# Kernel tuning notes

Hardware: AMD Instinct MI355X
Metric: run time of the kernel (lower is better)

## Reference

```python
import jax, jax.numpy as jnp
import numpy as np

K = 3

def setup_inputs() -> dict:
    key = jax.random.key(0)
    k1, k2, k3, k4 = jax.random.split(key, 4)
    B, N, F_in, T, F_out = 8, 2048, 16, 12, 32
    x = jax.random.normal(k1, (B, N, F_in, T), dtype=jnp.float32)
    spatial_attention = jax.random.uniform(k2, (B, N, N), dtype=jnp.float32)
    node_embeddings = jax.random.normal(k3, (N, 16), dtype=jnp.float32)
    theta = jax.random.normal(k4, (K, F_in, F_out), dtype=jnp.float32) * 0.1
    return {"x": x, "spatial_attention": spatial_attention,
            "node_embeddings": node_embeddings, "theta": theta}

def _cheb_polys(node_embeddings, N, K):
    # supports = softmax(relu(E E^T), axis=1)
    supports = jax.nn.softmax(jax.nn.relu(node_embeddings @ node_embeddings.T), axis=1)
    polys = [jnp.eye(N, dtype=supports.dtype), supports]
    for _ in range(2, K):
        polys.append(2.0 * supports @ polys[-1] - polys[-2])
    return jnp.stack(polys[:K], axis=0)  # (K, N, N)

def reference(x, spatial_attention, node_embeddings, theta):
    B, N, F_in, T = x.shape
    polys = _cheb_polys(node_embeddings, N, K)             # (K,N,N)
    # T_k_with_at = polys[k] * attention (broadcast over batch);
    # rhs = T_k_with_at^T @ graph_signal for every timestep:
    # (K,N,N)*(B,N,N) contracted with (B,N,F,T) over source node n -> (K,B,M,F,T)
    rhs = jnp.einsum('knm,bnm,bnft->kbmft', polys, spatial_attention, x)
    # accumulate rhs @ theta_k over k -> (B,M,F_out,T)
    out = jnp.einsum('kbmft,kfo->bmot', rhs, theta)
    return jax.nn.relu(out)
```

## Files before the change

### kernel.cpp

```cpp
#include <hip/hip_runtime.h>

#define NN    2048
#define BATCH 8
#define FIN   16
#define TT    12
#define FOUT  32
#define FT    (FIN*TT)
#define OT    (FOUT*TT)

typedef unsigned short ushort_t;
typedef __attribute__((ext_vector_type(8))) short   short8;
typedef __attribute__((ext_vector_type(4))) float   f32x4;
typedef __attribute__((ext_vector_type(4))) unsigned short us4;
typedef __attribute__((ext_vector_type(8))) unsigned short us8;

__device__ __forceinline__ float b2f(unsigned short u) {
    union { unsigned int i; float f; } v; v.i = ((unsigned int)u) << 16; return v.f;
}
__device__ __forceinline__ unsigned short f2b(float f) {
    union { float f; unsigned int i; } v; v.f = f;
    unsigned int x = v.i;
    x += 0x7fffu + ((x >> 16) & 1u);
    return (unsigned short)(x >> 16);
}

__global__ __launch_bounds__(256)
void k_supports(const float* __restrict__ E, ushort_t* __restrict__ Sb) {
    const int n = blockIdx.x;
    __shared__ float row[NN];
    __shared__ float red[256];
    const int tid = threadIdx.x;

    const f32x4 en0 = *(const f32x4*)&E[n * 16 + 0];
    const f32x4 en1 = *(const f32x4*)&E[n * 16 + 4];
    const f32x4 en2 = *(const f32x4*)&E[n * 16 + 8];
    const f32x4 en3 = *(const f32x4*)&E[n * 16 + 12];

    float lmax = 0.0f;
    for (int m = tid; m < NN; m += 256) {
        const f32x4* Em = (const f32x4*)&E[(size_t)m * 16];
        const f32x4 e0 = Em[0], e1 = Em[1], e2 = Em[2], e3 = Em[3];
        float d = 0.0f;
        #pragma unroll
        for (int j = 0; j < 4; ++j) d += en0[j] * e0[j];
        #pragma unroll
        for (int j = 0; j < 4; ++j) d += en1[j] * e1[j];
        #pragma unroll
        for (int j = 0; j < 4; ++j) d += en2[j] * e2[j];
        #pragma unroll
        for (int j = 0; j < 4; ++j) d += en3[j] * e3[j];
        d = fmaxf(d, 0.0f);
        row[m] = d;
        lmax = fmaxf(lmax, d);
    }
    red[tid] = lmax; __syncthreads();
    for (int s = 128; s > 0; s >>= 1) {
        if (tid < s) red[tid] = fmaxf(red[tid], red[tid + s]);
        __syncthreads();
    }
    const float mx = red[0];
    __syncthreads();

    float lsum = 0.0f;
    for (int m = tid; m < NN; m += 256) {
        float e = __expf(row[m] - mx);
        row[m] = e;
        lsum += e;
    }
    red[tid] = lsum; __syncthreads();
    for (int s = 128; s > 0; s >>= 1) {
        if (tid < s) red[tid] += red[tid + s];
        __syncthreads();
    }
    const float inv = 1.0f / red[0];
    for (int m = tid; m < NN; m += 256) Sb[(size_t)n * NN + m] = f2b(row[m] * inv);
}

__global__ __launch_bounds__(256)
void k_pack_st(const ushort_t* __restrict__ Sb, ushort_t* __restrict__ SbT) {
    const int r0 = blockIdx.x * 64, c0 = blockIdx.y * 64;
    __shared__ ushort_t Lt[64][65];
    const int tid = threadIdx.x;
    #pragma unroll
    for (int p = 0; p < 2; ++p) {
        const int i = (tid >> 3) + p * 32;
        const int j8 = (tid & 7) * 8;
        us8 v = *(const us8*)&Sb[(size_t)(r0 + i) * NN + c0 + j8];
        #pragma unroll
        for (int e = 0; e < 8; ++e) Lt[i][j8 + e] = v[e];
    }
    __syncthreads();
    #pragma unroll
    for (int p = 0; p < 2; ++p) {
        const int jj = (tid >> 3) + p * 32;
        const int i8 = (tid & 7) * 8;
        us8 v;
        #pragma unroll
        for (int e = 0; e < 8; ++e) v[e] = Lt[i8 + e][jj];
        *(us8*)&SbT[(size_t)(c0 + jj) * NN + r0 + i8] = v;
    }
}

__global__ __launch_bounds__(256)
void k_pack_x(const float* __restrict__ x, ushort_t* __restrict__ xbT) {
    const int nc = blockIdx.x * 64;
    const int b  = blockIdx.y;
    __shared__ ushort_t Lt[FT][65];
    const int tid = threadIdx.x;
    const float* __restrict__ xb = x + (size_t)b * NN * FT;
    #pragma unroll
    for (int p = 0; p < 12; ++p) {
        const int id = tid + 256 * p;
        const int nn = id / 48;
        const int f4 = (id % 48) * 4;
        const float4 v = *(const float4*)&xb[(size_t)(nc + nn) * FT + f4];
        Lt[f4 + 0][nn] = f2b(v.x);
        Lt[f4 + 1][nn] = f2b(v.y);
        Lt[f4 + 2][nn] = f2b(v.z);
        Lt[f4 + 3][nn] = f2b(v.w);
    }
    __syncthreads();
    #pragma unroll
    for (int p = 0; p < 6; ++p) {
        const int id = tid + 256 * p;
        const int ft = id >> 3;
        const int n8 = (id & 7) * 8;
        us8 v;
        #pragma unroll
        for (int e = 0; e < 8; ++e) v[e] = Lt[ft][n8 + e];
        *(us8*)&xbT[((size_t)b * FT + ft) * NN + nc + n8] = v;
    }
}

__global__ __launch_bounds__(256, 4)
void k_t2(const ushort_t* __restrict__ Sb, const ushort_t* __restrict__ SbT,
          ushort_t* __restrict__ T2b) {
    const int m0 = blockIdx.x * 64;
    const int n0 = blockIdx.y * 64;
    __shared__ __align__(16) ushort_t As[2][64 * 64];
    __shared__ __align__(16) ushort_t Bs[2][64 * 64];
    const int tid = threadIdx.x;
    const int lane = tid & 63, w = tid >> 6;
    const int l15 = lane & 15, q = lane >> 4, l7 = lane & 7;
    const int n0w = (w & 1) * 32, m0w = (w >> 1) * 32;
    const int sr = tid >> 3;
    const int sc = tid & 7;

    f32x4 acc[2][2];
    #pragma unroll
    for (int i = 0; i < 2; ++i)
        #pragma unroll
        for (int j = 0; j < 2; ++j) acc[i][j] = {0.f, 0.f, 0.f, 0.f};

    us8 avA[2], bvA[2], avB[2], bvB[2];

#define T2_LOAD(l0, av, bv)                                              \
    { _Pragma("unroll") for (int p = 0; p < 2; ++p) {                    \
        const int row_ = sr + 32 * p;                                    \
        av[p] = *(const us8*)&Sb[(size_t)(n0 + row_) * NN + (l0) + sc * 8];  \
        bv[p] = *(const us8*)&SbT[(size_t)(m0 + row_) * NN + (l0) + sc * 8]; \
      } }

#define T2_STORE(bufi, av, bv)                                           \
    { _Pragma("unroll") for (int p = 0; p < 2; ++p) {                    \
        const int row_ = sr + 32 * p;                                    \
        const int cs_ = (sc ^ (row_ & 7)) * 8;                           \
        *(us8*)&As[bufi][row_ * 64 + cs_] = av[p];                       \
        *(us8*)&Bs[bufi][row_ * 64 + cs_] = bv[p];                       \
      } }

#define T2_MFMA(bufi)                                                    \
    { _Pragma("unroll") for (int s = 0; s < 2; ++s) {                    \
        short8 a_[2], b_[2];                                             \
        const int u_ = ((s * 4 + q) ^ l7) * 8;                           \
        _Pragma("unroll") for (int i = 0; i < 2; ++i)                    \
            a_[i] = *(const short8*)&As[bufi][(n0w + i * 16 + l15) * 64 + u_]; \
        _Pragma("unroll") for (int j = 0; j < 2; ++j)                    \
            b_[j] = *(const short8*)&Bs[bufi][(m0w + j * 16 + l15) * 64 + u_]; \
        _Pragma("unroll") for (int i = 0; i < 2; ++i)                    \
            _Pragma("unroll") for (int j = 0; j < 2; ++j)                \
                acc[i][j] = __builtin_amdgcn_mfma_f32_16x16x32_bf16(a_[i], b_[j], acc[i][j], 0, 0, 0); \
      } }

    T2_LOAD(0, avA, bvA);
    T2_LOAD(64, avB, bvB);
    T2_STORE(0, avA, bvA);

    for (int it = 0; it < 32; it += 2) {
        __syncthreads();
        if (it < 30) T2_LOAD((it + 2) * 64, avA, bvA);
        T2_MFMA(0);
        T2_STORE(1, avB, bvB);
        __syncthreads();
        if (it < 29) T2_LOAD((it + 3) * 64, avB, bvB);
        T2_MFMA(1);
        if (it < 30) T2_STORE(0, avA, bvA);
    }
#undef T2_LOAD
#undef T2_STORE
#undef T2_MFMA

    #pragma unroll
    for (int i = 0; i < 2; ++i)
        #pragma unroll
        for (int j = 0; j < 2; ++j)
            #pragma unroll
            for (int r = 0; r < 4; ++r) {
                const int ng = n0 + n0w + i * 16 + q * 4 + r;
                const int mg = m0 + m0w + j * 16 + l15;
                const float v = 2.0f * acc[i][j][r] - (ng == mg ? 1.0f : 0.0f);
                T2b[(size_t)ng * NN + mg] = f2b(v);
            }
}

__global__ __launch_bounds__(256, 2)
void k_rhs(const ushort_t* __restrict__ Sb, const ushort_t* __restrict__ T2b,
           const float* __restrict__ att, const ushort_t* __restrict__ xbT,
           float* __restrict__ rhs) {
    const int m0 = blockIdx.x * 32;
    const int b  = blockIdx.y;
    __shared__ __align__(16) ushort_t As[2][2 * 32 * 64];
    __shared__ __align__(16) ushort_t Xs[2][FT * 64];
    const int tid = threadIdx.x;
    const int lane = tid & 63, w = tid >> 6;
    const int l15 = lane & 15, q = lane >> 4, l7 = lane & 7, l3 = lane >> 3;
    const int k1 = w & 1, ft0 = (w >> 1) * 96;
    const float* __restrict__ attb = att + (size_t)b * NN * NN;

    const int k1s = tid >> 7;
    const int uu  = tid & 127;
    const int m4  = (uu & 7) * 4;
    const int nn4 = (uu >> 3) * 4;
    const ushort_t* __restrict__ Pk = k1s ? T2b : Sb;

    f32x4 acc[2][6];
    #pragma unroll
    for (int i = 0; i < 2; ++i)
        #pragma unroll
        for (int t = 0; t < 6; ++t) acc[i][t] = {0.f, 0.f, 0.f, 0.f};

    us8   xvA[6], xvB[6];
    us4   pvA[4], pvB[4];
    f32x4 avA[4], avB[4];

#define RHS_LOAD(nc, xv, pv, av)                                         \
    { _Pragma("unroll") for (int p = 0; p < 6; ++p) {                    \
        const int row_ = (w * 6 + p) * 8 + l3;                           \
        xv[p] = *(const us8*)&xbT[((size_t)b * FT + row_) * NN + (nc) + l7 * 8]; \
      }                                                                  \
      _Pragma("unroll") for (int r = 0; r < 4; ++r) {                    \
        const int nn_ = (nc) + nn4 + r;                                  \
        pv[r] = *(const us4*)&Pk[(size_t)nn_ * NN + m0 + m4];            \
        av[r] = *(const f32x4*)&attb[(size_t)nn_ * NN + m0 + m4];        \
      } }

#define RHS_STORE(bufi, xv, pv, av)                                      \
    { _Pragma("unroll") for (int p = 0; p < 6; ++p) {                    \
        const int row_ = (w * 6 + p) * 8 + l3;                           \
        *(us8*)&Xs[bufi][row_ * 64 + (l7 ^ l3) * 8] = xv[p];             \
      }                                                                  \
      _Pragma("unroll") for (int c = 0; c < 4; ++c) {                    \
        const float w0_ = b2f(pv[0][c]) * av[0][c];                      \
        const float w1_ = b2f(pv[1][c]) * av[1][c];                      \
        const float w2_ = b2f(pv[2][c]) * av[2][c];                      \
        const float w3_ = b2f(pv[3][c]) * av[3][c];                      \
        unsigned int u01_, u23_;                                         \
        asm("v_cvt_pk_bf16_f32 %0, %1, %2" : "=v"(u01_) : "v"(w0_), "v"(w1_)); \
        asm("v_cvt_pk_bf16_f32 %0, %1, %2" : "=v"(u23_) : "v"(w2_), "v"(w3_)); \
        const int rowm_ = m4 + c;                                        \
        const int off_ = (((nn4 >> 3) ^ (rowm_ & 7)) * 8) + (nn4 & 4);   \
        *(uint2*)&As[bufi][(k1s * 32 + rowm_) * 64 + off_] = make_uint2(u01_, u23_); \
      } }

#define RHS_MFMA(bufi)                                                   \
    { _Pragma("unroll") for (int s = 0; s < 2; ++s) {                    \
        short8 a_[2], bb_[6];                                            \
        _Pragma("unroll") for (int i = 0; i < 2; ++i) {                  \
            const int row_ = i * 16 + l15;                               \
            a_[i] = *(const short8*)&As[bufi][(k1 * 32 + row_) * 64 + (((s * 4 + q) ^ l7) * 8)]; \
        }                                                                \
        _Pragma("unroll") for (int t = 0; t < 6; ++t) {                  \
            const int col_ = ft0 + t * 16 + l15;                         \
            const int u_ = ((s * 4 + q) ^ (col_ & 7)) * 8;               \
            bb_[t] = *(const short8*)&Xs[bufi][col_ * 64 + u_];          \
        }                                                                \
        _Pragma("unroll") for (int i = 0; i < 2; ++i)                    \
            _Pragma("unroll") for (int t = 0; t < 6; ++t)                \
                acc[i][t] = __builtin_amdgcn_mfma_f32_16x16x32_bf16(a_[i], bb_[t], acc[i][t], 0, 0, 0); \
      } }

    RHS_LOAD(0, xvA, pvA, avA);
    RHS_LOAD(64, xvB, pvB, avB);
    RHS_STORE(0, xvA, pvA, avA);

    for (int it = 0; it < 32; it += 2) {
        __syncthreads();
        if (it < 30) RHS_LOAD((it + 2) * 64, xvA, pvA, avA);
        RHS_MFMA(0);
        RHS_STORE(1, xvB, pvB, avB);
        __syncthreads();
        if (it < 29) RHS_LOAD((it + 3) * 64, xvB, pvB, avB);
        RHS_MFMA(1);
        if (it < 30) RHS_STORE(0, xvA, pvA, avA);
    }
#undef RHS_LOAD
#undef RHS_STORE
#undef RHS_MFMA

    float* __restrict__ op = rhs + ((size_t)(k1 * BATCH + b)) * NN * FT;
    #pragma unroll
    for (int i = 0; i < 2; ++i)
        #pragma unroll
        for (int t = 0; t < 6; ++t)
            #pragma unroll
            for (int r = 0; r < 4; ++r) {
                const int mg = m0 + i * 16 + q * 4 + r;
                const int ftg = ft0 + t * 16 + l15;
                op[(size_t)mg * FT + ftg] = acc[i][t][r];
            }
}

__global__ __launch_bounds__(128)
void k_out(const float* __restrict__ x, const float* __restrict__ att,
           const float* __restrict__ theta, const float* __restrict__ rhs,
           float* __restrict__ out) {
    const int m = blockIdx.x & (NN - 1);
    const int b = blockIdx.x >> 11;
    __shared__ float xr[FT], r1[FT], r2[FT];
    __shared__ float th[3 * FIN * FOUT];
    const int tid = threadIdx.x;

    const float* __restrict__ xb = x + ((size_t)b * NN + m) * FT;
    const float* __restrict__ p1 = rhs + ((size_t)0 * BATCH + b) * NN * FT + (size_t)m * FT;
    const float* __restrict__ p2 = rhs + ((size_t)1 * BATCH + b) * NN * FT + (size_t)m * FT;
    const float a0 = att[((size_t)b * NN + m) * NN + m];

    for (int i = tid; i < FT; i += 128) {
        xr[i] = xb[i] * a0;
        r1[i] = p1[i];
        r2[i] = p2[i];
    }
    for (int i = tid; i < 3 * FIN * FOUT; i += 128) th[i] = theta[i];
    __syncthreads();

    float* __restrict__ ob = out + ((size_t)b * NN + m) * OT;
    for (int idx = tid; idx < OT; idx += 128) {
        const int o = idx / TT, t = idx % TT;
        float acc = 0.0f;
        #pragma unroll
        for (int f = 0; f < FIN; ++f) {
            const int ft = f * TT + t;
            acc += th[f * FOUT + o] * xr[ft];
            acc += th[512 + f * FOUT + o] * r1[ft];
            acc += th[1024 + f * FOUT + o] * r2[ft];
        }
        ob[idx] = fmaxf(acc, 0.0f);
    }
}

extern "C" void kernel_launch(void* const* d_in, const int* in_sizes, int n_in,
                              void* d_out, int out_size, void* d_ws, size_t ws_size,
                              hipStream_t stream) {
    const float* x     = (const float*)d_in[0];
    const float* att   = (const float*)d_in[1];
    const float* E     = (const float*)d_in[2];
    const float* theta = (const float*)d_in[3];
    float* out = (float*)d_out;

    ushort_t* Sb  = (ushort_t*)d_ws;
    ushort_t* SbT = Sb  + (size_t)NN * NN;
    ushort_t* T2b = SbT + (size_t)NN * NN;
    ushort_t* xbT = T2b + (size_t)NN * NN;
    float*    rhs = (float*)(xbT + (size_t)BATCH * FT * NN);

    k_supports<<<NN, 256, 0, stream>>>(E, Sb);
    k_pack_st<<<dim3(32, 32), 256, 0, stream>>>(Sb, SbT);
    k_pack_x<<<dim3(32, BATCH), 256, 0, stream>>>(x, xbT);
    k_t2<<<dim3(32, 32), 256, 0, stream>>>(Sb, SbT, T2b);
    k_rhs<<<dim3(64, BATCH), 256, 0, stream>>>(Sb, T2b, att, xbT, rhs);
    k_out<<<BATCH * NN, 128, 0, stream>>>(x, att, theta, rhs, out);
}
```

Baseline: 338.7 us.

## Deepen GEMM software pipeline with explicit vmcnt waits and raw barriers

Restructures the double-buffered main loops of the T2 and RHS GEMM kernels so that two global loads stay in flight. The kernels now wait with explicit s_waitcnt vmcnt counts instead of relying on __syncthreads' full waits, and use s_barrier wrapped in sched_barrier. The aim is to overlap global-memory latency with MFMA work more aggressively. The risk is that the hard-coded vmcnt values must exactly match the number of loads each macro issues, or the code will read stale data.

```diff
diff --git a/kernel.cpp b/kernel.cpp
--- a/kernel.cpp
+++ b/kernel.cpp
@@ -23,6 +23,12 @@
     x += 0x7fffu + ((x >> 16) & 1u);
     return (unsigned short)(x >> 16);
 }
+
+#define VMWAIT(n) asm volatile("s_waitcnt vmcnt(" #n ")" ::: "memory")
+#define LGKM0()   asm volatile("s_waitcnt lgkmcnt(0)" ::: "memory")
+#define BAR()     do { __builtin_amdgcn_sched_barrier(0); \
+                       __builtin_amdgcn_s_barrier();      \
+                       __builtin_amdgcn_sched_barrier(0); } while (0)
 
 __global__ __launch_bounds__(256)
 void k_supports(const float* __restrict__ E, ushort_t* __restrict__ Sb) {
@@ -184,18 +190,22 @@
 
     T2_LOAD(0, avA, bvA);
     T2_LOAD(64, avB, bvB);
+    VMWAIT(4);
     T2_STORE(0, avA, bvA);
-
-    for (int it = 0; it < 32; it += 2) {
-        __syncthreads();
-        if (it < 30) T2_LOAD((it + 2) * 64, avA, bvA);
-        T2_MFMA(0);
-        T2_STORE(1, avB, bvB);
-        __syncthreads();
-        if (it < 29) T2_LOAD((it + 3) * 64, avB, bvB);
-        T2_MFMA(1);
-        if (it < 30) T2_STORE(0, avA, bvA);
-    }
+    T2_LOAD(128, avA, bvA);
+    LGKM0(); BAR();
+
+    for (int it = 0; it < 28; it += 2) {
+        T2_MFMA(0); VMWAIT(4); T2_STORE(1, avB, bvB);
+        T2_LOAD((it + 3) * 64, avB, bvB); LGKM0(); BAR();
+        T2_MFMA(1); VMWAIT(4); T2_STORE(0, avA, bvA);
+        T2_LOAD((it + 4) * 64, avA, bvA); LGKM0(); BAR();
+    }
+    T2_MFMA(0); VMWAIT(4); T2_STORE(1, avB, bvB);
+    T2_LOAD(31 * 64, avB, bvB); LGKM0(); BAR();
+    T2_MFMA(1); VMWAIT(4); T2_STORE(0, avA, bvA); LGKM0(); BAR();
+    T2_MFMA(0); VMWAIT(0); T2_STORE(1, avB, bvB); LGKM0(); BAR();
+    T2_MFMA(1);
 #undef T2_LOAD
 #undef T2_STORE
 #undef T2_MFMA
@@ -291,18 +301,22 @@
 
     RHS_LOAD(0, xvA, pvA, avA);
     RHS_LOAD(64, xvB, pvB, avB);
+    VMWAIT(14);
     RHS_STORE(0, xvA, pvA, avA);
-
-    for (int it = 0; it < 32; it += 2) {
-        __syncthreads();
-        if (it < 30) RHS_LOAD((it + 2) * 64, xvA, pvA, avA);
-        RHS_MFMA(0);
-        RHS_STORE(1, xvB, pvB, avB);
-        __syncthreads();
-        if (it < 29) RHS_LOAD((it + 3) * 64, xvB, pvB, avB);
-        RHS_MFMA(1);
-        if (it < 30) RHS_STORE(0, xvA, pvA, avA);
-    }
+    RHS_LOAD(128, xvA, pvA, avA);
+    LGKM0(); BAR();
+
+    for (int it = 0; it < 28; it += 2) {
+        RHS_MFMA(0); VMWAIT(14); RHS_STORE(1, xvB, pvB, avB);
+        RHS_LOAD((it + 3) * 64, xvB, pvB, avB); LGKM0(); BAR();
+        RHS_MFMA(1); VMWAIT(14); RHS_STORE(0, xvA, pvA, avA);
+        RHS_LOAD((it + 4) * 64, xvA, pvA, avA); LGKM0(); BAR();
+    }
+    RHS_MFMA(0); VMWAIT(14); RHS_STORE(1, xvB, pvB, avB);
+    RHS_LOAD(31 * 64, xvB, pvB, avB); LGKM0(); BAR();
+    RHS_MFMA(1); VMWAIT(14); RHS_STORE(0, xvA, pvA, avA); LGKM0(); BAR();
+    RHS_MFMA(0); VMWAIT(0); RHS_STORE(1, xvB, pvB, avB); LGKM0(); BAR();
+    RHS_MFMA(1);
 #undef RHS_LOAD
 #undef RHS_STORE
 #undef RHS_MFMA
```

Result: slower. 348.1 us (+2.8%).

## Widen k_rhs tile to 64 rows, single-buffer A, and use lighter barriers

Applied to the files above, without the earlier changes.

The k_rhs kernel now computes 64 output rows per block instead of 32, so each loaded X tile feeds twice as many MFMAs. The grid halves to 256 blocks. The A operand (polynomial times attention) is single-buffered and the loop is restructured so that A is written, then the next tile's loads are issued, then MFMA runs. Both k_t2 and k_rhs replace __syncthreads with an lgkmcnt wait plus a raw s_barrier. The larger accumulator and launch_bounds of 1 lower occupancy, and with fewer blocks the 256-CU device may be underfilled.

```diff
diff --git a/kernel.cpp b/kernel.cpp
--- a/kernel.cpp
+++ b/kernel.cpp
@@ -23,6 +23,9 @@
     x += 0x7fffu + ((x >> 16) & 1u);
     return (unsigned short)(x >> 16);
 }
+
+#define LGKM0()   asm volatile("s_waitcnt lgkmcnt(0)" ::: "memory")
+#define BARRIER() __builtin_amdgcn_s_barrier()
 
 __global__ __launch_bounds__(256)
 void k_supports(const float* __restrict__ E, ushort_t* __restrict__ Sb) {
@@ -187,11 +190,11 @@
     T2_STORE(0, avA, bvA);
 
     for (int it = 0; it < 32; it += 2) {
-        __syncthreads();
+        LGKM0(); BARRIER();
         if (it < 30) T2_LOAD((it + 2) * 64, avA, bvA);
         T2_MFMA(0);
         T2_STORE(1, avB, bvB);
-        __syncthreads();
+        LGKM0(); BARRIER();
         if (it < 29) T2_LOAD((it + 3) * 64, avB, bvB);
         T2_MFMA(1);
         if (it < 30) T2_STORE(0, avA, bvA);
@@ -213,13 +216,13 @@
             }
 }
 
-__global__ __launch_bounds__(256, 2)
+__global__ __launch_bounds__(256, 1)
 void k_rhs(const ushort_t* __restrict__ Sb, const ushort_t* __restrict__ T2b,
            const float* __restrict__ att, const ushort_t* __restrict__ xbT,
            float* __restrict__ rhs) {
-    const int m0 = blockIdx.x * 32;
+    const int m0 = blockIdx.x * 64;
     const int b  = blockIdx.y;
-    __shared__ __align__(16) ushort_t As[2][2 * 32 * 64];
+    __shared__ __align__(16) ushort_t As[128 * 64];
     __shared__ __align__(16) ushort_t Xs[2][FT * 64];
     const int tid = threadIdx.x;
     const int lane = tid & 63, w = tid >> 6;
@@ -229,87 +232,101 @@
 
     const int k1s = tid >> 7;
     const int uu  = tid & 127;
-    const int m4  = (uu & 7) * 4;
-    const int nn4 = (uu >> 3) * 4;
+    const int m4  = (uu & 15) * 4;
+    const int nn8 = (uu >> 4) * 8;
     const ushort_t* __restrict__ Pk = k1s ? T2b : Sb;
 
-    f32x4 acc[2][6];
-    #pragma unroll
-    for (int i = 0; i < 2; ++i)
+    f32x4 acc[4][6];
+    #pragma unroll
+    for (int i = 0; i < 4; ++i)
         #pragma unroll
         for (int t = 0; t < 6; ++t) acc[i][t] = {0.f, 0.f, 0.f, 0.f};
 
-    us8   xvA[6], xvB[6];
-    us4   pvA[4], pvB[4];
-    f32x4 avA[4], avB[4];
-
-#define RHS_LOAD(nc, xv, pv, av)                                         \
-    { _Pragma("unroll") for (int p = 0; p < 6; ++p) {                    \
-        const int row_ = (w * 6 + p) * 8 + l3;                           \
+    us8   xv[6];
+    us4   pv[8];
+    f32x4 av[8];
+
+#define RHS_LOADX(nc)                                                       \
+    { _Pragma("unroll") for (int p = 0; p < 6; ++p) {                       \
+        const int row_ = (w * 6 + p) * 8 + l3;                              \
         xv[p] = *(const us8*)&xbT[((size_t)b * FT + row_) * NN + (nc) + l7 * 8]; \
-      }                                                                  \
-      _Pragma("unroll") for (int r = 0; r < 4; ++r) {                    \
-        const int nn_ = (nc) + nn4 + r;                                  \
-        pv[r] = *(const us4*)&Pk[(size_t)nn_ * NN + m0 + m4];            \
-        av[r] = *(const f32x4*)&attb[(size_t)nn_ * NN + m0 + m4];        \
-      } }
-
-#define RHS_STORE(bufi, xv, pv, av)                                      \
-    { _Pragma("unroll") for (int p = 0; p < 6; ++p) {                    \
-        const int row_ = (w * 6 + p) * 8 + l3;                           \
-        *(us8*)&Xs[bufi][row_ * 64 + (l7 ^ l3) * 8] = xv[p];             \
-      }                                                                  \
-      _Pragma("unroll") for (int c = 0; c < 4; ++c) {                    \
-        const float w0_ = b2f(pv[0][c]) * av[0][c];                      \
-        const float w1_ = b2f(pv[1][c]) * av[1][c];                      \
-        const float w2_ = b2f(pv[2][c]) * av[2][c];                      \
-        const float w3_ = b2f(pv[3][c]) * av[3][c];                      \
-        unsigned int u01_, u23_;                                         \
-        asm("v_cvt_pk_bf16_f32 %0, %1, %2" : "=v"(u01_) : "v"(w0_), "v"(w1_)); \
-        asm("v_cvt_pk_bf16_f32 %0, %1, %2" : "=v"(u23_) : "v"(w2_), "v"(w3_)); \
-        const int rowm_ = m4 + c;                                        \
-        const int off_ = (((nn4 >> 3) ^ (rowm_ & 7)) * 8) + (nn4 & 4);   \
-        *(uint2*)&As[bufi][(k1s * 32 + rowm_) * 64 + off_] = make_uint2(u01_, u23_); \
-      } }
-
-#define RHS_MFMA(bufi)                                                   \
-    { _Pragma("unroll") for (int s = 0; s < 2; ++s) {                    \
-        short8 a_[2], bb_[6];                                            \
-        _Pragma("unroll") for (int i = 0; i < 2; ++i) {                  \
-            const int row_ = i * 16 + l15;                               \
-            a_[i] = *(const short8*)&As[bufi][(k1 * 32 + row_) * 64 + (((s * 4 + q) ^ l7) * 8)]; \
-        }                                                                \
-        _Pragma("unroll") for (int t = 0; t < 6; ++t) {                  \
-            const int col_ = ft0 + t * 16 + l15;                         \
-            const int u_ = ((s * 4 + q) ^ (col_ & 7)) * 8;               \
-            bb_[t] = *(const short8*)&Xs[bufi][col_ * 64 + u_];          \
-        }                                                                \
-        _Pragma("unroll") for (int i = 0; i < 2; ++i)                    \
-            _Pragma("unroll") for (int t = 0; t < 6; ++t)                \
+      } }
+
+#define RHS_LOADPA(nc)                                                      \
+    { _Pragma("unroll") for (int r = 0; r < 8; ++r) {                       \
+        const int nn_ = (nc) + nn8 + r;                                     \
+        pv[r] = *(const us4*)&Pk[(size_t)nn_ * NN + m0 + m4];               \
+        av[r] = *(const f32x4*)&attb[(size_t)nn_ * NN + m0 + m4];           \
+      } }
+
+#define RHS_WRITE_XS(bufi)                                                  \
+    { _Pragma("unroll") for (int p = 0; p < 6; ++p) {                       \
+        const int row_ = (w * 6 + p) * 8 + l3;                              \
+        *(us8*)&Xs[bufi][row_ * 64 + (l7 ^ l3) * 8] = xv[p];                \
+      } }
+
+#define RHS_WRITE_AS()                                                      \
+    { _Pragma("unroll") for (int c = 0; c < 4; ++c) {                       \
+        const int rowm_ = m4 + c;                                           \
+        const int g_ = (nn8 >> 3) ^ (rowm_ & 7);                            \
+        unsigned int u0_, u1_, u2_, u3_;                                    \
+        { const float a_ = b2f(pv[0][c]) * av[0][c];                        \
+          const float b_ = b2f(pv[1][c]) * av[1][c];                        \
+          asm("v_cvt_pk_bf16_f32 %0, %1, %2" : "=v"(u0_) : "v"(a_), "v"(b_)); } \
+        { const float a_ = b2f(pv[2][c]) * av[2][c];                        \
+          const float b_ = b2f(pv[3][c]) * av[3][c];                        \
+          asm("v_cvt_pk_bf16_f32 %0, %1, %2" : "=v"(u1_) : "v"(a_), "v"(b_)); } \
+        { const float a_ = b2f(pv[4][c]) * av[4][c];                        \
+          const float b_ = b2f(pv[5][c]) * av[5][c];                        \
+          asm("v_cvt_pk_bf16_f32 %0, %1, %2" : "=v"(u2_) : "v"(a_), "v"(b_)); } \
+        { const float a_ = b2f(pv[6][c]) * av[6][c];                        \
+          const float b_ = b2f(pv[7][c]) * av[7][c];                        \
+          asm("v_cvt_pk_bf16_f32 %0, %1, %2" : "=v"(u3_) : "v"(a_), "v"(b_)); } \
+        *(uint4*)&As[(k1s * 64 + rowm_) * 64 + g_ * 8] =                    \
+            make_uint4(u0_, u1_, u2_, u3_);                                 \
+      } }
+
+#define RHS_MFMA(bufi)                                                      \
+    { _Pragma("unroll") for (int s = 0; s < 2; ++s) {                       \
+        short8 a_[4], bb_[6];                                               \
+        _Pragma("unroll") for (int i = 0; i < 4; ++i) {                     \
+            const int rw_ = i * 16 + l15;                                   \
+            a_[i] = *(const short8*)&As[(k1 * 64 + rw_) * 64 + (((s * 4 + q) ^ l7) * 8)]; \
+        }                                                                   \
+        _Pragma("unroll") for (int t = 0; t < 6; ++t) {                     \
+            const int col_ = ft0 + t * 16 + l15;                            \
+            const int u_ = ((s * 4 + q) ^ (col_ & 7)) * 8;                  \
+            bb_[t] = *(const short8*)&Xs[bufi][col_ * 64 + u_];             \
+        }                                                                   \
+        _Pragma("unroll") for (int i = 0; i < 4; ++i)                       \
+            _Pragma("unroll") for (int t = 0; t < 6; ++t)                   \
                 acc[i][t] = __builtin_amdgcn_mfma_f32_16x16x32_bf16(a_[i], bb_[t], acc[i][t], 0, 0, 0); \
       } }
 
-    RHS_LOAD(0, xvA, pvA, avA);
-    RHS_LOAD(64, xvB, pvB, avB);
-    RHS_STORE(0, xvA, pvA, avA);
-
-    for (int it = 0; it < 32; it += 2) {
-        __syncthreads();
-        if (it < 30) RHS_LOAD((it + 2) * 64, xvA, pvA, avA);
-        RHS_MFMA(0);
-        RHS_STORE(1, xvB, pvB, avB);
-        __syncthreads();
-        if (it < 29) RHS_LOAD((it + 3) * 64, xvB, pvB, avB);
-        RHS_MFMA(1);
-        if (it < 30) RHS_STORE(0, xvA, pvA, avA);
-    }
-#undef RHS_LOAD
-#undef RHS_STORE
+    RHS_LOADX(0);
+    RHS_LOADPA(0);
+    RHS_WRITE_XS(0);
+
+    for (int c = 0; c < 32; ++c) {
+        LGKM0(); BARRIER();
+        RHS_WRITE_AS();
+        if (c < 31) {
+            RHS_LOADX((c + 1) * 64);
+            RHS_LOADPA((c + 1) * 64);
+        }
+        LGKM0(); BARRIER();
+        RHS_MFMA(c & 1);
+        if (c < 31) RHS_WRITE_XS((c + 1) & 1);
+    }
+#undef RHS_LOADX
+#undef RHS_LOADPA
+#undef RHS_WRITE_XS
+#undef RHS_WRITE_AS
 #undef RHS_MFMA
 
     float* __restrict__ op = rhs + ((size_t)(k1 * BATCH + b)) * NN * FT;
     #pragma unroll
-    for (int i = 0; i < 2; ++i)
+    for (int i = 0; i < 4; ++i)
         #pragma unroll
         for (int t = 0; t < 6; ++t)
             #pragma unroll
@@ -377,6 +394,6 @@
     k_pack_st<<<dim3(32, 32), 256, 0, stream>>>(Sb, SbT);
     k_pack_x<<<dim3(32, BATCH), 256, 0, stream>>>(x, xbT);
     k_t2<<<dim3(32, 32), 256, 0, stream>>>(Sb, SbT, T2b);
-    k_rhs<<<dim3(64, BATCH), 256, 0, stream>>>(Sb, T2b, att, xbT, rhs);
+    k_rhs<<<dim3(32, BATCH), 256, 0, stream>>>(Sb, T2b, att, xbT, rhs);
     k_out<<<BATCH * NN, 128, 0, stream>>>(x, att, theta, rhs, out);
 }
```

Measured after the change: 331.6 us. -2.1%, faster.
